# Kernel tuning notes

Hardware: AMD Instinct MI355X
Metric: run time of the kernel (lower is better)

The kernel has to match this reference:

```python
import jax, jax.numpy as jnp
import numpy as np
from jax import lax

ALPHA = 0.1  # leak rate dt/tau
T, B, NIN, N, NOUT = 1024, 64, 32, 256, 16


def setup_inputs() -> dict:
    key = jax.random.key(0)
    ks = jax.random.split(key, 6)
    inputs = jax.random.normal(ks[0], (T, B, NIN), dtype=jnp.float32)
    noise = jax.random.normal(ks[1], (T, B, N), dtype=jnp.float32)
    x0 = jax.random.normal(ks[2], (B, N), dtype=jnp.float32)
    Win = jax.random.normal(ks[3], (NIN, N), dtype=jnp.float32) / np.sqrt(NIN)
    Wrec = jax.random.normal(ks[4], (N, N), dtype=jnp.float32) / np.sqrt(N)
    brec = jnp.zeros((N,), dtype=jnp.float32)
    Wout = jax.random.normal(ks[5], (N, NOUT), dtype=jnp.float32) / np.sqrt(N)
    bout = jnp.zeros((NOUT,), dtype=jnp.float32)
    return {"inputs": inputs, "noise": noise, "x0": x0, "Win": Win,
            "Wrec": Wrec, "brec": brec, "Wout": Wout, "bout": bout}


def reference(inputs, noise, x0, Win, Wrec, brec, Wout, bout):
    """Leaky vanilla RNN over T steps.
    x_t = (1-a)*x_{t-1} + a*(u_t@Win + tanh(x_{t-1})@Wrec + brec) + q_t
    z_t = tanh(x_t)@Wout + bout
    Returns (outputs [T,B,Nout], states [T,B,N]).
    """
    def step(x_tm1, uq):
        u_t, q_t = uq
        r_tm1 = jnp.tanh(x_tm1)
        x_t = (1.0 - ALPHA) * x_tm1 + ALPHA * (
            u_t @ Win + r_tm1 @ Wrec + brec) + q_t
        z_t = jnp.tanh(x_t) @ Wout + bout
        return x_t, (z_t, x_t)

    _, (outputs, states) = lax.scan(step, x0, (inputs, noise))
    return outputs, states
```

## Files before the change

kernel.cpp:

```cpp
#include <hip/hip_runtime.h>

#define T_STEPS 1024
#define BATCH   64
#define NIN     32
#define NH      256
#define NOUT    16

typedef __attribute__((ext_vector_type(8))) _Float16 half8;
typedef __attribute__((ext_vector_type(4))) _Float16 half4;
typedef __attribute__((ext_vector_type(4))) float    f32x4;

__device__ __forceinline__ float fast_tanh(float x) {
  float e = __builtin_amdgcn_exp2f(x * 2.8853900817779268f);
  return 1.0f - 2.0f * __builtin_amdgcn_rcpf(e + 1.0f);
}

#define ROW 320
#define BUFSZ (16 * 320)


__global__ __launch_bounds__(512, 2)
void RecurrentNetwork_19628000543215_kernel(
    const float* __restrict__ inputs,
    const float* __restrict__ noise,
    const float* __restrict__ x0,
    const float* __restrict__ Win,
    const float* __restrict__ Wrec,
    const float* __restrict__ brec,
    float* __restrict__ outx)
{
  __shared__ alignas(16) unsigned short rlds[2 * BUFSZ];

  const int g   = blockIdx.x;
  const int tid = threadIdx.x;
  const int w   = tid >> 6;
  const int l   = tid & 63;
  const int m   = l & 15;
  const int q   = l >> 4;
  const int b   = 16 * g + m;
  const int mx  = m & 7;

  half8 wr[2][9];
  int   ldso[9];
  #pragma unroll
  for (int i = 0; i < 9; ++i) {
    int kt = w + i; if (kt >= 9) kt -= 9;
    ldso[i] = m * ROW + ((((4 * kt + q) ^ mx)) << 3);
    #pragma unroll
    for (int nt = 0; nt < 2; ++nt) {
      const int n = 32 * w + 16 * nt + m;
      #pragma unroll
      for (int j = 0; j < 8; ++j) {
        const int k = 32 * kt + 8 * q + j;
        const float v = (kt < 8) ? Wrec[(size_t)k * NH + n]
                                 : Win[(size_t)(k - 256) * NH + n];
        wr[nt][i][j] = (_Float16)(0.1f * v);
      }
    }
  }

  f32x4 brecs[2], x[2];
  #pragma unroll
  for (int nt = 0; nt < 2; ++nt) {
    const int n0 = 32 * w + 16 * nt + 4 * q;
    brecs[nt] = 0.1f * (*(const f32x4*)(brec + n0));
    x[nt]     = *(const f32x4*)(x0 + (size_t)b * NH + n0);
  }

  #pragma unroll
  for (int nt = 0; nt < 2; ++nt) {
    const int n0 = 32 * w + 16 * nt + 4 * q;
    half4 r;
    r.x = (_Float16)fast_tanh(x[nt].x);
    r.y = (_Float16)fast_tanh(x[nt].y);
    r.z = (_Float16)fast_tanh(x[nt].z);
    r.w = (_Float16)fast_tanh(x[nt].w);
    const int blk = (n0 >> 3) ^ mx;
    *(half4*)&rlds[m * ROW + blk * 8 + (n0 & 7)] = r;
  }
  if (w == 1) {
    const float* up = inputs + (size_t)b * NIN + 8 * q;
    const f32x4 ua = *(const f32x4*)up;
    const f32x4 ub = *(const f32x4*)(up + 4);
    half8 uu;
    uu[0]=(_Float16)ua.x; uu[1]=(_Float16)ua.y; uu[2]=(_Float16)ua.z; uu[3]=(_Float16)ua.w;
    uu[4]=(_Float16)ub.x; uu[5]=(_Float16)ub.y; uu[6]=(_Float16)ub.z; uu[7]=(_Float16)ub.w;
    const int blk = (32 + q) ^ mx;
    *(half8*)&rlds[m * ROW + blk * 8] = uu;
  }
  f32x4 qv[2];
  qv[0] = *(const f32x4*)(noise + (size_t)b * NH + 32 * w + 4 * q);
  qv[1] = *(const f32x4*)(noise + (size_t)b * NH + 32 * w + 16 + 4 * q);
  __syncthreads();

  half8 bfw = *(const half8*)&rlds[ldso[0]];

  const float* np = noise  + (size_t)BATCH * NH  + (size_t)b * NH  + 32 * w + 4 * q;
  const float* ip = inputs + (size_t)BATCH * NIN + (size_t)b * NIN + 8 * q;
  float*       xp = outx   + (size_t)b * NH + 32 * w + 4 * q;

  #pragma unroll 1
  for (int t = 0; t < T_STEPS; ++t) {
    const int rb = (t & 1) * BUFSZ;
    const int wb = BUFSZ - rb;

    f32x4 ua, ub;
    if (w == 1) {
      ua = *(const f32x4*)ip;
      ub = *(const f32x4*)(ip + 4);
    }
    const f32x4 qn0 = *(const f32x4*)np;
    const f32x4 qn1 = *(const f32x4*)(np + 16);

    f32x4 accA[2], accB[2];
    accA[0] = brecs[0]; accA[1] = brecs[1];
    accB[0] = f32x4{0.f, 0.f, 0.f, 0.f};
    accB[1] = f32x4{0.f, 0.f, 0.f, 0.f};

    accA[0] = __builtin_amdgcn_mfma_f32_16x16x32_f16(wr[0][0], bfw, accA[0], 0, 0, 0);
    accA[1] = __builtin_amdgcn_mfma_f32_16x16x32_f16(wr[1][0], bfw, accA[1], 0, 0, 0);
    #pragma unroll
    for (int i = 1; i < 9; ++i) {
      const half8 bf = *(const half8*)&rlds[rb + ldso[i]];
      if (i & 1) {
        accB[0] = __builtin_amdgcn_mfma_f32_16x16x32_f16(wr[0][i], bf, accB[0], 0, 0, 0);
        accB[1] = __builtin_amdgcn_mfma_f32_16x16x32_f16(wr[1][i], bf, accB[1], 0, 0, 0);
      } else {
        accA[0] = __builtin_amdgcn_mfma_f32_16x16x32_f16(wr[0][i], bf, accA[0], 0, 0, 0);
        accA[1] = __builtin_amdgcn_mfma_f32_16x16x32_f16(wr[1][i], bf, accA[1], 0, 0, 0);
      }
    }

    x[0] = 0.9f * x[0] + (accA[0] + accB[0]) + qv[0];
    x[1] = 0.9f * x[1] + (accA[1] + accB[1]) + qv[1];

    #pragma unroll
    for (int nt = 0; nt < 2; ++nt) {
      const int n0 = 32 * w + 16 * nt + 4 * q;
      half4 r;
#if __has_builtin(__builtin_amdgcn_cvt_pkrtz)
      {
        auto plo = __builtin_amdgcn_cvt_pkrtz(fast_tanh(x[nt].x), fast_tanh(x[nt].y));
        auto phi = __builtin_amdgcn_cvt_pkrtz(fast_tanh(x[nt].z), fast_tanh(x[nt].w));
        r.x = plo.x; r.y = plo.y; r.z = phi.x; r.w = phi.y;
      }
#else
      r.x = (_Float16)fast_tanh(x[nt].x);
      r.y = (_Float16)fast_tanh(x[nt].y);
      r.z = (_Float16)fast_tanh(x[nt].z);
      r.w = (_Float16)fast_tanh(x[nt].w);
#endif
      const int blk = (n0 >> 3) ^ mx;
      *(half4*)&rlds[wb + m * ROW + blk * 8 + (n0 & 7)] = r;
    }

    if (w == 1) {
      half8 uu;
      uu[0]=(_Float16)ua.x; uu[1]=(_Float16)ua.y; uu[2]=(_Float16)ua.z; uu[3]=(_Float16)ua.w;
      uu[4]=(_Float16)ub.x; uu[5]=(_Float16)ub.y; uu[6]=(_Float16)ub.z; uu[7]=(_Float16)ub.w;
      const int blk = (32 + q) ^ mx;
      *(half8*)&rlds[wb + m * ROW + blk * 8] = uu;
    }

    asm volatile("" ::: "memory");
    bfw = *(const half8*)&rlds[wb + ldso[0]];

    *(f32x4*)(xp)      = x[0];
    *(f32x4*)(xp + 16) = x[1];
    qv[0] = qn0; qv[1] = qn1;
    const bool adv = (t <= T_STEPS - 3);
    np += adv ? (size_t)(BATCH * NH)  : (size_t)0;
    ip += adv ? (size_t)(BATCH * NIN) : (size_t)0;
    xp += (size_t)(BATCH * NH);

    asm volatile("s_waitcnt lgkmcnt(0)" ::: "memory");
    __builtin_amdgcn_s_barrier();
    asm volatile("" ::: "memory");
  }
}

__global__ __launch_bounds__(256, 4)
void RecurrentNetwork_19628000543215_zkernel(
    const float* __restrict__ states,
    const float* __restrict__ Wout,
    const float* __restrict__ bout,
    float* __restrict__ outz)
{
  const int tid  = threadIdx.x;
  const int wv   = tid >> 6;
  const int l    = tid & 63;
  const int m    = l & 15;
  const int q    = l >> 4;
  const int tile = blockIdx.x * 4 + wv;
  const int row  = tile * 16 + m;

  half8 wo[8];
  #pragma unroll
  for (int kt = 0; kt < 8; ++kt)
    #pragma unroll
    for (int j = 0; j < 8; ++j)
      wo[kt][j] = (_Float16)Wout[(size_t)(32 * kt + 8 * q + j) * NOUT + m];

  f32x4 zac = *(const f32x4*)(bout + 4 * q);
  const float* xrow = states + (size_t)row * NH;

  #pragma unroll
  for (int kt = 0; kt < 8; ++kt) {
    const f32x4 xa = *(const f32x4*)(xrow + 32 * kt + 8 * q);
    const f32x4 xb = *(const f32x4*)(xrow + 32 * kt + 8 * q + 4);
    half8 rf;
    rf[0] = (_Float16)fast_tanh(xa.x);
    rf[1] = (_Float16)fast_tanh(xa.y);
    rf[2] = (_Float16)fast_tanh(xa.z);
    rf[3] = (_Float16)fast_tanh(xa.w);
    rf[4] = (_Float16)fast_tanh(xb.x);
    rf[5] = (_Float16)fast_tanh(xb.y);
    rf[6] = (_Float16)fast_tanh(xb.z);
    rf[7] = (_Float16)fast_tanh(xb.w);
    zac = __builtin_amdgcn_mfma_f32_16x16x32_f16(wo[kt], rf, zac, 0, 0, 0);
  }
  *(f32x4*)(outz + (size_t)row * NOUT + 4 * q) = zac;
}

extern "C" void kernel_launch(void* const* d_in, const int* in_sizes, int n_in,
                              void* d_out, int out_size, void* d_ws, size_t ws_size,
                              hipStream_t stream) {
  (void)in_sizes; (void)n_in; (void)out_size; (void)d_ws; (void)ws_size;
  float* outz = (float*)d_out;
  float* outx = (float*)d_out + (size_t)T_STEPS * BATCH * NOUT;
  RecurrentNetwork_19628000543215_kernel<<<dim3(4), dim3(512), 0, stream>>>(
      (const float*)d_in[0],
      (const float*)d_in[1],
      (const float*)d_in[2],
      (const float*)d_in[3],
      (const float*)d_in[4],
      (const float*)d_in[5],
      outx);
  RecurrentNetwork_19628000543215_zkernel<<<dim3(1024), dim3(256), 0, stream>>>(
      outx,
      (const float*)d_in[6],
      (const float*)d_in[7],
      outz);
}
```

Before: 1.175 ms.

## Precompute input projection and noise in a parallel kernel before the recurrence

Adds a fully parallel kernel that computes 0.1*(u_t@Win + brec) + q_t for all timesteps with MFMA and writes it into the states output buffer. The sequential recurrent kernel then seeds its accumulators from this precomputed term and overwrites it in place with x_t. This drops the Win k-tile from the per-step MFMA chain (9 to 8 tiles) and removes the per-step input loads and LDS staging. The cost is an extra launch plus a full read/write pass over a noise-sized tensor, and in-place reuse of the output buffer depends on each step reading its row before that row is overwritten.

After: 1.095 ms. 6.8% less time.

```diff
diff --git a/kernel.cpp b/kernel.cpp
--- a/kernel.cpp
+++ b/kernel.cpp
@@ -19,14 +19,57 @@
 #define BUFSZ (16 * 320)
 
 
+__global__ __launch_bounds__(256, 2)
+void RecurrentNetwork_19628000543215_ukernel(
+    const float* __restrict__ inputs,
+    const float* __restrict__ noise,
+    const float* __restrict__ Win,
+    const float* __restrict__ brec,
+    float* __restrict__ U)
+{
+  const int tid = threadIdx.x;
+  const int wv  = tid >> 6;
+  const int l   = tid & 63;
+  const int m   = l & 15;
+  const int q   = l >> 4;
+
+  half8 wf[16];
+  f32x4 bs[16];
+  #pragma unroll
+  for (int nt = 0; nt < 16; ++nt) {
+    #pragma unroll
+    for (int j = 0; j < 8; ++j)
+      wf[nt][j] = (_Float16)(0.1f * Win[(size_t)(8 * q + j) * NH + 16 * nt + m]);
+    bs[nt] = 0.1f * (*(const f32x4*)(brec + 16 * nt + 4 * q));
+  }
+
+  #pragma unroll
+  for (int s = 0; s < 2; ++s) {
+    const int tile = blockIdx.x * 4 + wv + s * 2048;
+    const int row  = tile * 16 + m;
+    const float* up = inputs + (size_t)row * NIN + 8 * q;
+    const f32x4 ua = *(const f32x4*)up;
+    const f32x4 ub = *(const f32x4*)(up + 4);
+    half8 uf;
+    uf[0]=(_Float16)ua.x; uf[1]=(_Float16)ua.y; uf[2]=(_Float16)ua.z; uf[3]=(_Float16)ua.w;
+    uf[4]=(_Float16)ub.x; uf[5]=(_Float16)ub.y; uf[6]=(_Float16)ub.z; uf[7]=(_Float16)ub.w;
+
+    const float* qp = noise + (size_t)row * NH;
+    float*       Up = U     + (size_t)row * NH;
+    #pragma unroll
+    for (int nt = 0; nt < 16; ++nt) {
+      f32x4 acc = bs[nt] + *(const f32x4*)(qp + 16 * nt + 4 * q);
+      acc = __builtin_amdgcn_mfma_f32_16x16x32_f16(wf[nt], uf, acc, 0, 0, 0);
+      *(f32x4*)(Up + 16 * nt + 4 * q) = acc;
+    }
+  }
+}
+
 __global__ __launch_bounds__(512, 2)
 void RecurrentNetwork_19628000543215_kernel(
-    const float* __restrict__ inputs,
-    const float* __restrict__ noise,
+    const float* __restrict__ Uu,
     const float* __restrict__ x0,
-    const float* __restrict__ Win,
     const float* __restrict__ Wrec,
-    const float* __restrict__ brec,
     float* __restrict__ outx)
 {
   __shared__ alignas(16) unsigned short rlds[2 * BUFSZ];
@@ -40,11 +83,11 @@
   const int b   = 16 * g + m;
   const int mx  = m & 7;
 
-  half8 wr[2][9];
-  int   ldso[9];
-  #pragma unroll
-  for (int i = 0; i < 9; ++i) {
-    int kt = w + i; if (kt >= 9) kt -= 9;
+  half8 wr[2][8];
+  int   ldso[8];
+  #pragma unroll
+  for (int i = 0; i < 8; ++i) {
+    const int kt = (w + i) & 7;
     ldso[i] = m * ROW + ((((4 * kt + q) ^ mx)) << 3);
     #pragma unroll
     for (int nt = 0; nt < 2; ++nt) {
@@ -52,20 +95,15 @@
       #pragma unroll
       for (int j = 0; j < 8; ++j) {
         const int k = 32 * kt + 8 * q + j;
-        const float v = (kt < 8) ? Wrec[(size_t)k * NH + n]
-                                 : Win[(size_t)(k - 256) * NH + n];
-        wr[nt][i][j] = (_Float16)(0.1f * v);
+        wr[nt][i][j] = (_Float16)(0.1f * Wrec[(size_t)k * NH + n]);
       }
     }
   }
 
-  f32x4 brecs[2], x[2];
-  #pragma unroll
-  for (int nt = 0; nt < 2; ++nt) {
-    const int n0 = 32 * w + 16 * nt + 4 * q;
-    brecs[nt] = 0.1f * (*(const f32x4*)(brec + n0));
-    x[nt]     = *(const f32x4*)(x0 + (size_t)b * NH + n0);
-  }
+  f32x4 x[2];
+  #pragma unroll
+  for (int nt = 0; nt < 2; ++nt)
+    x[nt] = *(const f32x4*)(x0 + (size_t)b * NH + 32 * w + 16 * nt + 4 * q);
 
   #pragma unroll
   for (int nt = 0; nt < 2; ++nt) {
@@ -78,49 +116,33 @@
     const int blk = (n0 >> 3) ^ mx;
     *(half4*)&rlds[m * ROW + blk * 8 + (n0 & 7)] = r;
   }
-  if (w == 1) {
-    const float* up = inputs + (size_t)b * NIN + 8 * q;
-    const f32x4 ua = *(const f32x4*)up;
-    const f32x4 ub = *(const f32x4*)(up + 4);
-    half8 uu;
-    uu[0]=(_Float16)ua.x; uu[1]=(_Float16)ua.y; uu[2]=(_Float16)ua.z; uu[3]=(_Float16)ua.w;
-    uu[4]=(_Float16)ub.x; uu[5]=(_Float16)ub.y; uu[6]=(_Float16)ub.z; uu[7]=(_Float16)ub.w;
-    const int blk = (32 + q) ^ mx;
-    *(half8*)&rlds[m * ROW + blk * 8] = uu;
-  }
   f32x4 qv[2];
-  qv[0] = *(const f32x4*)(noise + (size_t)b * NH + 32 * w + 4 * q);
-  qv[1] = *(const f32x4*)(noise + (size_t)b * NH + 32 * w + 16 + 4 * q);
+  qv[0] = *(const f32x4*)(Uu + (size_t)b * NH + 32 * w + 4 * q);
+  qv[1] = *(const f32x4*)(Uu + (size_t)b * NH + 32 * w + 16 + 4 * q);
   __syncthreads();
 
   half8 bfw = *(const half8*)&rlds[ldso[0]];
 
-  const float* np = noise  + (size_t)BATCH * NH  + (size_t)b * NH  + 32 * w + 4 * q;
-  const float* ip = inputs + (size_t)BATCH * NIN + (size_t)b * NIN + 8 * q;
-  float*       xp = outx   + (size_t)b * NH + 32 * w + 4 * q;
+  const float* np = Uu   + (size_t)BATCH * NH + (size_t)b * NH + 32 * w + 4 * q;
+  float*       xp = outx + (size_t)b * NH + 32 * w + 4 * q;
 
   #pragma unroll 1
   for (int t = 0; t < T_STEPS; ++t) {
     const int rb = (t & 1) * BUFSZ;
     const int wb = BUFSZ - rb;
 
-    f32x4 ua, ub;
-    if (w == 1) {
-      ua = *(const f32x4*)ip;
-      ub = *(const f32x4*)(ip + 4);
-    }
     const f32x4 qn0 = *(const f32x4*)np;
     const f32x4 qn1 = *(const f32x4*)(np + 16);
 
     f32x4 accA[2], accB[2];
-    accA[0] = brecs[0]; accA[1] = brecs[1];
+    accA[0] = qv[0]; accA[1] = qv[1];
     accB[0] = f32x4{0.f, 0.f, 0.f, 0.f};
     accB[1] = f32x4{0.f, 0.f, 0.f, 0.f};
 
     accA[0] = __builtin_amdgcn_mfma_f32_16x16x32_f16(wr[0][0], bfw, accA[0], 0, 0, 0);
     accA[1] = __builtin_amdgcn_mfma_f32_16x16x32_f16(wr[1][0], bfw, accA[1], 0, 0, 0);
     #pragma unroll
-    for (int i = 1; i < 9; ++i) {
+    for (int i = 1; i < 8; ++i) {
       const half8 bf = *(const half8*)&rlds[rb + ldso[i]];
       if (i & 1) {
         accB[0] = __builtin_amdgcn_mfma_f32_16x16x32_f16(wr[0][i], bf, accB[0], 0, 0, 0);
@@ -131,35 +153,18 @@
       }
     }
 
-    x[0] = 0.9f * x[0] + (accA[0] + accB[0]) + qv[0];
-    x[1] = 0.9f * x[1] + (accA[1] + accB[1]) + qv[1];
+    x[0] = 0.9f * x[0] + (accA[0] + accB[0]);
+    x[1] = 0.9f * x[1] + (accA[1] + accB[1]);
 
     #pragma unroll
     for (int nt = 0; nt < 2; ++nt) {
       const int n0 = 32 * w + 16 * nt + 4 * q;
       half4 r;
-#if __has_builtin(__builtin_amdgcn_cvt_pkrtz)
-      {
-        auto plo = __builtin_amdgcn_cvt_pkrtz(fast_tanh(x[nt].x), fast_tanh(x[nt].y));
-        auto phi = __builtin_amdgcn_cvt_pkrtz(fast_tanh(x[nt].z), fast_tanh(x[nt].w));
-        r.x = plo.x; r.y = plo.y; r.z = phi.x; r.w = phi.y;
-      }
-#else
-      r.x = (_Float16)fast_tanh(x[nt].x);
-      r.y = (_Float16)fast_tanh(x[nt].y);
-      r.z = (_Float16)fast_tanh(x[nt].z);
-      r.w = (_Float16)fast_tanh(x[nt].w);
-#endif
+      auto plo = __builtin_amdgcn_cvt_pkrtz(fast_tanh(x[nt].x), fast_tanh(x[nt].y));
+      auto phi = __builtin_amdgcn_cvt_pkrtz(fast_tanh(x[nt].z), fast_tanh(x[nt].w));
+      r.x = plo.x; r.y = plo.y; r.z = phi.x; r.w = phi.y;
       const int blk = (n0 >> 3) ^ mx;
       *(half4*)&rlds[wb + m * ROW + blk * 8 + (n0 & 7)] = r;
-    }
-
-    if (w == 1) {
-      half8 uu;
-      uu[0]=(_Float16)ua.x; uu[1]=(_Float16)ua.y; uu[2]=(_Float16)ua.z; uu[3]=(_Float16)ua.w;
-      uu[4]=(_Float16)ub.x; uu[5]=(_Float16)ub.y; uu[6]=(_Float16)ub.z; uu[7]=(_Float16)ub.w;
-      const int blk = (32 + q) ^ mx;
-      *(half8*)&rlds[wb + m * ROW + blk * 8] = uu;
     }
 
     asm volatile("" ::: "memory");
@@ -169,8 +174,7 @@
     *(f32x4*)(xp + 16) = x[1];
     qv[0] = qn0; qv[1] = qn1;
     const bool adv = (t <= T_STEPS - 3);
-    np += adv ? (size_t)(BATCH * NH)  : (size_t)0;
-    ip += adv ? (size_t)(BATCH * NIN) : (size_t)0;
+    np += adv ? (size_t)(BATCH * NH) : (size_t)0;
     xp += (size_t)(BATCH * NH);
 
     asm volatile("s_waitcnt lgkmcnt(0)" ::: "memory");
@@ -228,13 +232,16 @@
   (void)in_sizes; (void)n_in; (void)out_size; (void)d_ws; (void)ws_size;
   float* outz = (float*)d_out;
   float* outx = (float*)d_out + (size_t)T_STEPS * BATCH * NOUT;
-  RecurrentNetwork_19628000543215_kernel<<<dim3(4), dim3(512), 0, stream>>>(
+  RecurrentNetwork_19628000543215_ukernel<<<dim3(512), dim3(256), 0, stream>>>(
       (const float*)d_in[0],
       (const float*)d_in[1],
+      (const float*)d_in[3],
+      (const float*)d_in[5],
+      outx);
+  RecurrentNetwork_19628000543215_kernel<<<dim3(4), dim3(512), 0, stream>>>(
+      outx,
       (const float*)d_in[2],
-      (const float*)d_in[3],
       (const float*)d_in[4],
-      (const float*)d_in[5],
       outx);
   RecurrentNetwork_19628000543215_zkernel<<<dim3(1024), dim3(256), 0, stream>>>(
       outx,
```
